# Optimization experiments

Hardware: AMD Instinct MI355X
Metric: run time of the kernel (lower is better)

The kernel has to match this reference:

```python
import math
import jax, jax.numpy as jnp
import numpy as np

B, L, D, H, DK = 2, 2048, 1024, 16, 64
LATTICE = (4, 4)


def _build_neighbours(n_heads, shape):
    positions = [divmod(i, shape[1]) for i in range(n_heads)]
    idx = np.full((n_heads, 8), -1, dtype=np.int32)
    w = np.zeros((n_heads, 8), dtype=np.float32)
    for i, (r1, c1) in enumerate(positions):
        k = 0
        for dr in (-1, 0, 1):
            for dc in (-1, 0, 1):
                if dr == 0 and dc == 0:
                    continue
                if k >= 8:
                    break
                tgt = (r1 + dr, c1 + dc)
                for j, p in enumerate(positions):
                    if p == tgt:
                        idx[i, k] = j
                        w[i, k] = math.exp(-math.hypot(dr, dc))
                        k += 1
                        break
    return idx, w


def setup_inputs() -> dict:
    key = jax.random.key(0)
    ks = jax.random.split(key, 8)
    s = 1.0 / math.sqrt(D)  # typical linear init scale
    nb_idx, nb_w = _build_neighbours(H, LATTICE)
    return {
        "query": jax.random.normal(ks[0], (B, L, D), jnp.float32),
        "key": jax.random.normal(ks[1], (B, L, D), jnp.float32),
        "value": jax.random.normal(ks[2], (B, L, D), jnp.float32),
        "Wq": jax.random.normal(ks[3], (H, DK, D), jnp.float32) * s,
        "Wk": jax.random.normal(ks[4], (H, DK, D), jnp.float32) * s,
        "Wv": jax.random.normal(ks[5], (H, DK, D), jnp.float32) * s,
        "coupling_strength": jnp.full((H,), 0.1, jnp.float32),
        "out_w": jax.random.normal(ks[6], (D, D), jnp.float32) * s,
        "out_b": jnp.zeros((D,), jnp.float32),
        "neighbour_w": jnp.asarray(nb_w),
        "mask": jax.random.randint(ks[7], (B, L), 0, 2, jnp.int32),
        "neighbour_idx": jnp.asarray(nb_idx),
    }


def _phases(coupling_strength, neighbour_idx, neighbour_w):
    # Sequential Kuramoto update over heads (order matters: earlier heads'
    # updated phases are visible to later heads, as in the torch loop).
    freq = 1.0 + 0.1 * jnp.arange(H, dtype=jnp.float32)
    ph = jnp.zeros((H,), jnp.float32)
    two_pi = 2.0 * math.pi
    for i in range(H):  # H=16, structurally distinct sequential states
        nb = jnp.clip(neighbour_idx[i], 0, H - 1)  # invalid slots have w==0
        coupling = jnp.sum(neighbour_w[i] * jnp.sin(ph[nb] - ph[i]))
        new = jnp.mod(ph[i] + 0.01 * (freq[i] + coupling_strength[i] * coupling), two_pi)
        ph = ph.at[i].set(new)
    return ph


def reference(query, key, value, Wq, Wk, Wv, coupling_strength, out_w, out_b,
              neighbour_w, mask, neighbour_idx):
    ph = _phases(coupling_strength, neighbour_idx, neighbour_w)
    bias = 0.1 * jnp.cos(ph)  # [H] per-head scalar bias

    # Batched per-head projections: [B,L,D] x [H,DK,D] -> [B,H,L,DK]
    Q = jnp.einsum('bld,hkd->bhlk', query, Wq)
    K = jnp.einsum('bld,hkd->bhlk', key, Wk)
    V = jnp.einsum('bld,hkd->bhlk', value, Wv)

    scale = math.sqrt(float(DK))
    scores = jnp.einsum('bhqd,bhkd->bhqk', Q, K) / scale  # [B,H,L,L]
    scores = scores + bias[None, :, None, None]
    m = mask[:, None, None, :]  # [B,1,1,L], matches mask.unsqueeze(1).unsqueeze(1)
    scores = jnp.where(m == 0, jnp.float32(-10000.0), scores)
    attn = jax.nn.softmax(scores, axis=-1)
    out = jnp.einsum('bhqk,bhkd->bhqd', attn, V)  # [B,H,L,DK]
    out = out.transpose(0, 2, 1, 3).reshape(B, L, H * DK)  # concat heads
    return out @ out_w.T + out_b
```

## Files before the change

### kernel.cpp

```cpp
#include <hip/hip_runtime.h>
#include <hip/hip_fp16.h>


#define B_ 2
#define L_ 2048
#define D_ 1024
#define H_ 16
#define DK_ 64

#define QSCALE 0.1803368801111244f
#define MASKOFF -14427.0f

typedef _Float16 f16;
typedef _Float16 f16x2 __attribute__((ext_vector_type(2)));
typedef _Float16 f16x4 __attribute__((ext_vector_type(4)));
typedef _Float16 f16x8 __attribute__((ext_vector_type(8)));
typedef __fp16 hf16x2 __attribute__((ext_vector_type(2)));
typedef float f32x4 __attribute__((ext_vector_type(4)));

static __device__ __forceinline__ float fast_exp2(float x) {
    float r;
    asm("v_exp_f32 %0, %1" : "=v"(r) : "v"(x));
    return r;
}

__global__ __launch_bounds__(256) void qkv_proj_kernel(
    const float* __restrict__ query, const float* __restrict__ keyx,
    const float* __restrict__ value,
    const float* __restrict__ Wq, const float* __restrict__ Wk,
    const float* __restrict__ Wv,
    f16* __restrict__ Qh, f16* __restrict__ Kh, f16* __restrict__ VhT)
{
    const int z = blockIdx.z;
    const float* X = (z == 0) ? query : (z == 1) ? keyx : value;
    const float* W = (z == 0) ? Wq : (z == 1) ? Wk : Wv;
    f16* out = (z == 0) ? Qh : (z == 1) ? Kh : VhT;
    const float qs = (z == 0) ? QSCALE : 1.0f;

    const int m0 = blockIdx.x * 128;
    const int n0 = blockIdx.y * 128;
    const int tid = threadIdx.x;
    const int lane = tid & 63;
    const int w = tid >> 6;
    const int wr = (w >> 1) * 64, wc = (w & 1) * 64;

    __shared__ f16 As[128 * 40];
    __shared__ f16 Ws[128 * 40];

    f32x4 acc[4][4] = {};

    const int r = tid >> 3, c = (tid & 7) * 4;
    float4 ra[4], rb[4];

    auto issueK = [&](int kk) {
        #pragma unroll
        for (int p = 0; p < 4; ++p) {
            ra[p] = *(const float4*)&X[(size_t)(m0 + p * 32 + r) * D_ + kk + c];
            rb[p] = *(const float4*)&W[(size_t)(n0 + p * 32 + r) * D_ + kk + c];
        }
    };
    auto storeK = [&]() {
        #pragma unroll
        for (int p = 0; p < 4; ++p) {
            int row = p * 32 + r;
            f16x4 ha = { (f16)(ra[p].x * qs), (f16)(ra[p].y * qs),
                         (f16)(ra[p].z * qs), (f16)(ra[p].w * qs) };
            *(f16x4*)&As[row * 40 + c] = ha;
            f16x4 hb = { (f16)rb[p].x, (f16)rb[p].y, (f16)rb[p].z, (f16)rb[p].w };
            *(f16x4*)&Ws[row * 40 + c] = hb;
        }
    };

    issueK(0);
    for (int kk = 0; kk < D_; kk += 32) {
        __syncthreads();
        storeK();
        if (kk + 32 < D_) issueK(kk + 32);
        __syncthreads();

        f16x8 af[4], bf[4];
        const int lg = (lane >> 4) * 8;
        #pragma unroll
        for (int i = 0; i < 4; ++i) {
            af[i] = *(const f16x8*)&As[(wr + i * 16 + (lane & 15)) * 40 + lg];
            bf[i] = *(const f16x8*)&Ws[(wc + i * 16 + (lane & 15)) * 40 + lg];
        }
        #pragma unroll
        for (int i = 0; i < 4; ++i)
            #pragma unroll
            for (int j = 0; j < 4; ++j)
                acc[i][j] = __builtin_amdgcn_mfma_f32_16x16x32_f16(af[i], bf[j], acc[i][j], 0, 0, 0);
    }

    if (z == 2) {
        #pragma unroll
        for (int i = 0; i < 4; ++i) {
            int grow = m0 + wr + i * 16 + (lane >> 4) * 4;
            int b = grow >> 11, l = grow & (L_ - 1);
            #pragma unroll
            for (int j = 0; j < 4; ++j) {
                int gcol = n0 + wc + j * 16 + (lane & 15);
                int hh = gcol >> 6, k = gcol & 63;
                f16x4 o = { (f16)acc[i][j][0], (f16)acc[i][j][1],
                            (f16)acc[i][j][2], (f16)acc[i][j][3] };
                *(f16x4*)&out[((size_t)((b * H_ + hh) * DK_ + k)) * L_ + l] = o;
            }
        }
    } else {
        #pragma unroll
        for (int i = 0; i < 4; ++i) {
            int grow = m0 + wr + i * 16 + (lane >> 4) * 4;
            #pragma unroll
            for (int j = 0; j < 4; ++j) {
                int gcol = n0 + wc + j * 16 + (lane & 15);
                int hh = gcol >> 6, k = gcol & 63;
                #pragma unroll
                for (int rr = 0; rr < 4; ++rr) {
                    int row = grow + rr;
                    int b = row >> 11, l = row & (L_ - 1);
                    out[(((size_t)(b * H_ + hh)) * L_ + l) * DK_ + k] = (f16)acc[i][j][rr];
                }
            }
        }
    }
}

__global__ __launch_bounds__(256) void attn_kernel(
    const f16* __restrict__ Qh, const f16* __restrict__ Kh,
    const f16* __restrict__ VhT, const int* __restrict__ mask,
    f16* __restrict__ Oh)
{
    const int n = blockIdx.x;
    const int bh = ((n >> 7) << 3) + (n & 7);
    const int qb = (n >> 3) & 15;
    const int b = bh >> 4, h = bh & 15;
    const int q0 = qb * 128;
    const int tid = threadIdx.x;
    const int lane = tid & 63;
    const int w = tid >> 6;
    const int lq = lane & 15, g = lane >> 4;

    __shared__ f16 Ks[2][64 * 72];
    __shared__ f16 Vt[2][64 * 72];
    __shared__ f16 Plds[4][32 * 72];
    __shared__ float mofft[2][64];

    const size_t base = (size_t)bh * L_ * DK_;
    const int* maskp = mask + b * L_;

    f16x8 qf0[2], qf1[2];
    {
        const f16* qptr = Qh + base + (size_t)(q0 + w * 32 + lq) * DK_ + g * 8;
        qf0[0] = *(const f16x8*)(qptr);
        qf0[1] = *(const f16x8*)(qptr + 32);
        qptr += 16 * DK_;
        qf1[0] = *(const f16x8*)(qptr);
        qf1[1] = *(const f16x8*)(qptr + 32);
    }

    const int srow = tid >> 2, scol = (tid & 3) * 16;

    f32x4 acc0[4] = {}, acc1[4] = {};
    float mrun0 = -1e30f, lrun0 = 0.f;
    float mrun1 = -1e30f, lrun1 = 0.f;

    f16x8 kr0, kr1, vr0, vr1;

    auto issue = [&](int k0) {
        const f16* kp = Kh + base + (size_t)(k0 + srow) * DK_ + scol;
        kr0 = *(const f16x8*)kp;
        kr1 = *(const f16x8*)(kp + 8);
        const f16* vp = VhT + (size_t)(bh * DK_ + srow) * L_ + k0 + scol;
        vr0 = *(const f16x8*)vp;
        vr1 = *(const f16x8*)(vp + 8);
    };

    auto store_tile = [&](int buf, int k0) {
        *(f16x8*)&Ks[buf][srow * 72 + scol] = kr0;
        *(f16x8*)&Ks[buf][srow * 72 + scol + 8] = kr1;
        *(f16x8*)&Vt[buf][srow * 72 + scol] = vr0;
        *(f16x8*)&Vt[buf][srow * 72 + scol + 8] = vr1;
        if (tid < 16) {
            int4 mv = *(const int4*)&maskp[k0 + tid * 4];
            float4 f = { mv.x ? 0.f : MASKOFF, mv.y ? 0.f : MASKOFF,
                         mv.z ? 0.f : MASKOFF, mv.w ? 0.f : MASKOFF };
            *(float4*)&mofft[buf][tid * 4] = f;
        }
    };

    auto softmax_store = [&](float* sv, float& mrun, float& lrun,
                             f32x4* acc, int rowoff) {
        float a0 = fmaxf(sv[0], sv[1]),  a1 = fmaxf(sv[2], sv[3]);
        float a2 = fmaxf(sv[4], sv[5]),  a3 = fmaxf(sv[6], sv[7]);
        float a4 = fmaxf(sv[8], sv[9]),  a5 = fmaxf(sv[10], sv[11]);
        float a6 = fmaxf(sv[12], sv[13]), a7 = fmaxf(sv[14], sv[15]);
        float m = fmaxf(fmaxf(fmaxf(a0, a1), fmaxf(a2, a3)),
                        fmaxf(fmaxf(a4, a5), fmaxf(a6, a7)));
        m = fmaxf(m, __shfl_xor(m, 16, 64));
        m = fmaxf(m, __shfl_xor(m, 32, 64));
        if (__any(m > mrun)) {
            float mn = fmaxf(mrun, m);
            float scl = fast_exp2(mrun - mn);
            mrun = mn;
            lrun *= scl;
            #pragma unroll
            for (int f = 0; f < 4; ++f) acc[f] *= scl;
        }
        f16* pl = (f16*)Plds[w];
        float ls0 = 0.f, ls1 = 0.f;
        #pragma unroll
        for (int kt = 0; kt < 4; ++kt) {
            float p0 = fast_exp2(sv[kt * 4 + 0] - mrun);
            float p1 = fast_exp2(sv[kt * 4 + 1] - mrun);
            float p2 = fast_exp2(sv[kt * 4 + 2] - mrun);
            float p3 = fast_exp2(sv[kt * 4 + 3] - mrun);
            ls0 += p0 + p1;
            ls1 += p2 + p3;
            hf16x2 lo = __builtin_amdgcn_cvt_pkrtz(p0, p1);
            hf16x2 hi = __builtin_amdgcn_cvt_pkrtz(p2, p3);
            f16x2 lo2 = __builtin_bit_cast(f16x2, lo);
            f16x2 hi2 = __builtin_bit_cast(f16x2, hi);
            f16x4 pk; pk[0] = lo2[0]; pk[1] = lo2[1]; pk[2] = hi2[0]; pk[3] = hi2[1];
            *(f16x4*)&pl[(rowoff + lq) * 72 + kt * 16 + g * 4] = pk;
        }
        lrun += ls0 + ls1;
    };

    auto compute = [&](int buf) {
        float sv0[16], sv1[16];
        __builtin_amdgcn_s_setprio(1);
        #pragma unroll
        for (int kt = 0; kt < 4; ++kt) {
            f32x4 cin = *(const f32x4*)&mofft[buf][kt * 16 + g * 4];
            const f16* ka = &Ks[buf][(kt * 16 + lq) * 72 + g * 8];
            f16x8 a0 = *(const f16x8*)ka;
            f16x8 a1 = *(const f16x8*)(ka + 32);
            f32x4 s0 = __builtin_amdgcn_mfma_f32_16x16x32_f16(a0, qf0[0], cin, 0, 0, 0);
            s0 = __builtin_amdgcn_mfma_f32_16x16x32_f16(a1, qf0[1], s0, 0, 0, 0);
            f32x4 s1 = __builtin_amdgcn_mfma_f32_16x16x32_f16(a0, qf1[0], cin, 0, 0, 0);
            s1 = __builtin_amdgcn_mfma_f32_16x16x32_f16(a1, qf1[1], s1, 0, 0, 0);
            *(f32x4*)&sv0[kt * 4] = s0;
            *(f32x4*)&sv1[kt * 4] = s1;
        }
        __builtin_amdgcn_s_setprio(0);

        softmax_store(sv0, mrun0, lrun0, acc0, 0);
        softmax_store(sv1, mrun1, lrun1, acc1, 16);
        asm volatile("s_waitcnt lgkmcnt(0)" ::: "memory");
        __builtin_amdgcn_sched_barrier(0);

        f16* pl = (f16*)Plds[w];
        __builtin_amdgcn_s_setprio(1);
        #pragma unroll
        for (int kc = 0; kc < 2; ++kc) {
            f16x8 pb0 = *(const f16x8*)&pl[lq * 72 + kc * 32 + g * 8];
            f16x8 pb1 = *(const f16x8*)&pl[(16 + lq) * 72 + kc * 32 + g * 8];
            #pragma unroll
            for (int f = 0; f < 4; ++f) {
                f16x8 va = *(const f16x8*)&Vt[buf][(f * 16 + lq) * 72 + kc * 32 + g * 8];
                acc0[f] = __builtin_amdgcn_mfma_f32_16x16x32_f16(va, pb0, acc0[f], 0, 0, 0);
                acc1[f] = __builtin_amdgcn_mfma_f32_16x16x32_f16(va, pb1, acc1[f], 0, 0, 0);
            }
        }
        __builtin_amdgcn_s_setprio(0);
    };

    issue(0);
    store_tile(0, 0);
    issue(64);
    __syncthreads();

    #pragma unroll 2
    for (int t = 0; t < 32; ++t) {
        int buf = t & 1;
        if (t + 1 < 32) store_tile(buf ^ 1, (t + 1) * 64);
        if (t + 2 < 32) issue((t + 2) * 64);
        compute(buf);
        __syncthreads();
    }

    lrun0 += __shfl_xor(lrun0, 16, 64);
    lrun0 += __shfl_xor(lrun0, 32, 64);
    lrun1 += __shfl_xor(lrun1, 16, 64);
    lrun1 += __shfl_xor(lrun1, 32, 64);
    {
        float inv = 1.f / lrun0;
        int q = q0 + w * 32 + lq;
        #pragma unroll
        for (int f = 0; f < 4; ++f) {
            f16x4 o = { (f16)(acc0[f][0] * inv), (f16)(acc0[f][1] * inv),
                        (f16)(acc0[f][2] * inv), (f16)(acc0[f][3] * inv) };
            *(f16x4*)&Oh[((size_t)(b * L_ + q)) * D_ + h * 64 + f * 16 + g * 4] = o;
        }
    }
    {
        float inv = 1.f / lrun1;
        int q = q0 + w * 32 + 16 + lq;
        #pragma unroll
        for (int f = 0; f < 4; ++f) {
            f16x4 o = { (f16)(acc1[f][0] * inv), (f16)(acc1[f][1] * inv),
                        (f16)(acc1[f][2] * inv), (f16)(acc1[f][3] * inv) };
            *(f16x4*)&Oh[((size_t)(b * L_ + q)) * D_ + h * 64 + f * 16 + g * 4] = o;
        }
    }
}

__global__ __launch_bounds__(256) void out_proj_kernel(
    const f16* __restrict__ Oh, const float* __restrict__ outw,
    const float* __restrict__ outb, float* __restrict__ Y)
{
    const int m0 = blockIdx.x * 128;
    const int n0 = blockIdx.y * 128;
    const int tid = threadIdx.x;
    const int lane = tid & 63;
    const int w = tid >> 6;
    const int wr = (w >> 1) * 64, wc = (w & 1) * 64;

    __shared__ f16 As[128 * 40];
    __shared__ f16 Ws[128 * 40];

    f32x4 acc[4][4] = {};

    const int r = tid >> 3, c = (tid & 7) * 4;
    f16x4 ra[4];
    float4 rb[4];

    auto issueK = [&](int kk) {
        #pragma unroll
        for (int p = 0; p < 4; ++p) {
            ra[p] = *(const f16x4*)&Oh[(size_t)(m0 + p * 32 + r) * D_ + kk + c];
            rb[p] = *(const float4*)&outw[(size_t)(n0 + p * 32 + r) * D_ + kk + c];
        }
    };
    auto storeK = [&]() {
        #pragma unroll
        for (int p = 0; p < 4; ++p) {
            int row = p * 32 + r;
            *(f16x4*)&As[row * 40 + c] = ra[p];
            f16x4 hb = { (f16)rb[p].x, (f16)rb[p].y, (f16)rb[p].z, (f16)rb[p].w };
            *(f16x4*)&Ws[row * 40 + c] = hb;
        }
    };

    issueK(0);
    for (int kk = 0; kk < D_; kk += 32) {
        __syncthreads();
        storeK();
        if (kk + 32 < D_) issueK(kk + 32);
        __syncthreads();

        f16x8 af[4], bf[4];
        const int lg = (lane >> 4) * 8;
        #pragma unroll
        for (int i = 0; i < 4; ++i) {
            af[i] = *(const f16x8*)&As[(wr + i * 16 + (lane & 15)) * 40 + lg];
            bf[i] = *(const f16x8*)&Ws[(wc + i * 16 + (lane & 15)) * 40 + lg];
        }
        #pragma unroll
        for (int i = 0; i < 4; ++i)
            #pragma unroll
            for (int j = 0; j < 4; ++j)
                acc[i][j] = __builtin_amdgcn_mfma_f32_16x16x32_f16(af[i], bf[j], acc[i][j], 0, 0, 0);
    }

    #pragma unroll
    for (int i = 0; i < 4; ++i) {
        int grow = m0 + wr + i * 16 + (lane >> 4) * 4;
        #pragma unroll
        for (int j = 0; j < 4; ++j) {
            int gcol = n0 + wc + j * 16 + (lane & 15);
            float bias = outb[gcol];
            #pragma unroll
            for (int rr = 0; rr < 4; ++rr)
                Y[(size_t)(grow + rr) * D_ + gcol] = acc[i][j][rr] + bias;
        }
    }
}

extern "C" void kernel_launch(void* const* d_in, const int* in_sizes, int n_in,
                              void* d_out, int out_size, void* d_ws, size_t ws_size,
                              hipStream_t stream) {
    const float* query = (const float*)d_in[0];
    const float* key   = (const float*)d_in[1];
    const float* value = (const float*)d_in[2];
    const float* Wq    = (const float*)d_in[3];
    const float* Wk    = (const float*)d_in[4];
    const float* Wv    = (const float*)d_in[5];
    const float* outw  = (const float*)d_in[7];
    const float* outb  = (const float*)d_in[8];
    const int*   mask  = (const int*)d_in[10];
    float* Y = (float*)d_out;

    char* ws = (char*)d_ws;
    f16* Qh  = (f16*)(ws);
    f16* Kh  = (f16*)(ws + 8388608);
    f16* VhT = (f16*)(ws + 16777216);
    f16* Oh  = (f16*)(ws + 25165824);

    qkv_proj_kernel<<<dim3(32, 8, 3), 256, 0, stream>>>(query, key, value,
                                                        Wq, Wk, Wv, Qh, Kh, VhT);
    attn_kernel<<<dim3(512), 256, 0, stream>>>(Qh, Kh, VhT, mask, Oh);
    out_proj_kernel<<<dim3(32, 8), 256, 0, stream>>>(Oh, outw, outb, Y);
}
```

Baseline: 149.9 us.

## Double-buffer LDS in projection GEMMs and swap MFMA operands for vector stores

The QKV projection and output projection GEMMs now use two LDS buffers, so each k-step needs one barrier instead of two and the next tile's store overlaps the current compute. The MFMA operands are swapped for row-major outputs, which transposes the accumulator layout so each lane holds four consecutive columns. The epilogue can then write f16x4 or float4 vectors instead of scalar stores. The cost is twice the LDS per block, which may lower occupancy.

After: 154.8 us. 1.03x slower.

```diff
diff --git a/kernel.cpp b/kernel.cpp
--- a/kernel.cpp
+++ b/kernel.cpp
@@ -44,8 +44,8 @@
     const int w = tid >> 6;
     const int wr = (w >> 1) * 64, wc = (w & 1) * 64;
 
-    __shared__ f16 As[128 * 40];
-    __shared__ f16 Ws[128 * 40];
+    __shared__ f16 As[2][128 * 40];
+    __shared__ f16 Ws[2][128 * 40];
 
     f32x4 acc[4][4] = {};
 
@@ -59,37 +59,52 @@
             rb[p] = *(const float4*)&W[(size_t)(n0 + p * 32 + r) * D_ + kk + c];
         }
     };
-    auto storeK = [&]() {
+    auto storeK = [&](int buf) {
         #pragma unroll
         for (int p = 0; p < 4; ++p) {
             int row = p * 32 + r;
             f16x4 ha = { (f16)(ra[p].x * qs), (f16)(ra[p].y * qs),
                          (f16)(ra[p].z * qs), (f16)(ra[p].w * qs) };
-            *(f16x4*)&As[row * 40 + c] = ha;
+            *(f16x4*)&As[buf][row * 40 + c] = ha;
             f16x4 hb = { (f16)rb[p].x, (f16)rb[p].y, (f16)rb[p].z, (f16)rb[p].w };
-            *(f16x4*)&Ws[row * 40 + c] = hb;
-        }
-    };
-
-    issueK(0);
-    for (int kk = 0; kk < D_; kk += 32) {
-        __syncthreads();
-        storeK();
-        if (kk + 32 < D_) issueK(kk + 32);
-        __syncthreads();
-
+            *(f16x4*)&Ws[buf][row * 40 + c] = hb;
+        }
+    };
+
+    auto computeK = [&](int buf) {
         f16x8 af[4], bf[4];
         const int lg = (lane >> 4) * 8;
         #pragma unroll
         for (int i = 0; i < 4; ++i) {
-            af[i] = *(const f16x8*)&As[(wr + i * 16 + (lane & 15)) * 40 + lg];
-            bf[i] = *(const f16x8*)&Ws[(wc + i * 16 + (lane & 15)) * 40 + lg];
-        }
-        #pragma unroll
-        for (int i = 0; i < 4; ++i)
-            #pragma unroll
-            for (int j = 0; j < 4; ++j)
-                acc[i][j] = __builtin_amdgcn_mfma_f32_16x16x32_f16(af[i], bf[j], acc[i][j], 0, 0, 0);
+            af[i] = *(const f16x8*)&As[buf][(wr + i * 16 + (lane & 15)) * 40 + lg];
+            bf[i] = *(const f16x8*)&Ws[buf][(wc + i * 16 + (lane & 15)) * 40 + lg];
+        }
+        if (z == 2) {
+            #pragma unroll
+            for (int i = 0; i < 4; ++i)
+                #pragma unroll
+                for (int j = 0; j < 4; ++j)
+                    acc[i][j] = __builtin_amdgcn_mfma_f32_16x16x32_f16(af[i], bf[j], acc[i][j], 0, 0, 0);
+        } else {
+            #pragma unroll
+            for (int i = 0; i < 4; ++i)
+                #pragma unroll
+                for (int j = 0; j < 4; ++j)
+                    acc[i][j] = __builtin_amdgcn_mfma_f32_16x16x32_f16(bf[j], af[i], acc[i][j], 0, 0, 0);
+        }
+    };
+
+    issueK(0);
+    storeK(0);
+    issueK(32);
+    __syncthreads();
+
+    for (int t = 0; t < 32; ++t) {
+        int buf = t & 1;
+        if (t + 1 < 32) storeK(buf ^ 1);
+        if (t + 2 < 32) issueK((t + 2) * 32);
+        computeK(buf);
+        __syncthreads();
     }
 
     if (z == 2) {
@@ -109,17 +124,15 @@
     } else {
         #pragma unroll
         for (int i = 0; i < 4; ++i) {
-            int grow = m0 + wr + i * 16 + (lane >> 4) * 4;
+            int m = m0 + wr + i * 16 + (lane & 15);
+            int b = m >> 11, l = m & (L_ - 1);
             #pragma unroll
             for (int j = 0; j < 4; ++j) {
-                int gcol = n0 + wc + j * 16 + (lane & 15);
-                int hh = gcol >> 6, k = gcol & 63;
-                #pragma unroll
-                for (int rr = 0; rr < 4; ++rr) {
-                    int row = grow + rr;
-                    int b = row >> 11, l = row & (L_ - 1);
-                    out[(((size_t)(b * H_ + hh)) * L_ + l) * DK_ + k] = (f16)acc[i][j][rr];
-                }
+                int nn = n0 + wc + j * 16 + (lane >> 4) * 4;
+                int hh = nn >> 6, k = nn & 63;
+                f16x4 o = { (f16)acc[i][j][0], (f16)acc[i][j][1],
+                            (f16)acc[i][j][2], (f16)acc[i][j][3] };
+                *(f16x4*)&out[(((size_t)(b * H_ + hh)) * L_ + l) * DK_ + k] = o;
             }
         }
     }
@@ -316,8 +329,8 @@
     const int w = tid >> 6;
     const int wr = (w >> 1) * 64, wc = (w & 1) * 64;
 
-    __shared__ f16 As[128 * 40];
-    __shared__ f16 Ws[128 * 40];
+    __shared__ f16 As[2][128 * 40];
+    __shared__ f16 Ws[2][128 * 40];
 
     f32x4 acc[4][4] = {};
 
@@ -332,47 +345,54 @@
             rb[p] = *(const float4*)&outw[(size_t)(n0 + p * 32 + r) * D_ + kk + c];
         }
     };
-    auto storeK = [&]() {
+    auto storeK = [&](int buf) {
         #pragma unroll
         for (int p = 0; p < 4; ++p) {
             int row = p * 32 + r;
-            *(f16x4*)&As[row * 40 + c] = ra[p];
+            *(f16x4*)&As[buf][row * 40 + c] = ra[p];
             f16x4 hb = { (f16)rb[p].x, (f16)rb[p].y, (f16)rb[p].z, (f16)rb[p].w };
-            *(f16x4*)&Ws[row * 40 + c] = hb;
-        }
-    };
-
-    issueK(0);
-    for (int kk = 0; kk < D_; kk += 32) {
-        __syncthreads();
-        storeK();
-        if (kk + 32 < D_) issueK(kk + 32);
-        __syncthreads();
-
+            *(f16x4*)&Ws[buf][row * 40 + c] = hb;
+        }
+    };
+
+    auto computeK = [&](int buf) {
         f16x8 af[4], bf[4];
         const int lg = (lane >> 4) * 8;
         #pragma unroll
         for (int i = 0; i < 4; ++i) {
-            af[i] = *(const f16x8*)&As[(wr + i * 16 + (lane & 15)) * 40 + lg];
-            bf[i] = *(const f16x8*)&Ws[(wc + i * 16 + (lane & 15)) * 40 + lg];
+            af[i] = *(const f16x8*)&As[buf][(wr + i * 16 + (lane & 15)) * 40 + lg];
+            bf[i] = *(const f16x8*)&Ws[buf][(wc + i * 16 + (lane & 15)) * 40 + lg];
         }
         #pragma unroll
         for (int i = 0; i < 4; ++i)
             #pragma unroll
             for (int j = 0; j < 4; ++j)
-                acc[i][j] = __builtin_amdgcn_mfma_f32_16x16x32_f16(af[i], bf[j], acc[i][j], 0, 0, 0);
+                acc[i][j] = __builtin_amdgcn_mfma_f32_16x16x32_f16(bf[j], af[i], acc[i][j], 0, 0, 0);
+    };
+
+    issueK(0);
+    storeK(0);
+    issueK(32);
+    __syncthreads();
+
+    for (int t = 0; t < 32; ++t) {
+        int buf = t & 1;
+        if (t + 1 < 32) storeK(buf ^ 1);
+        if (t + 2 < 32) issueK((t + 2) * 32);
+        computeK(buf);
+        __syncthreads();
     }
 
     #pragma unroll
     for (int i = 0; i < 4; ++i) {
-        int grow = m0 + wr + i * 16 + (lane >> 4) * 4;
+        int m = m0 + wr + i * 16 + (lane & 15);
         #pragma unroll
         for (int j = 0; j < 4; ++j) {
-            int gcol = n0 + wc + j * 16 + (lane & 15);
-            float bias = outb[gcol];
-            #pragma unroll
-            for (int rr = 0; rr < 4; ++rr)
-                Y[(size_t)(grow + rr) * D_ + gcol] = acc[i][j][rr] + bias;
+            int nn = n0 + wc + j * 16 + (lane >> 4) * 4;
+            float4 bias = *(const float4*)&outb[nn];
+            float4 o = { acc[i][j][0] + bias.x, acc[i][j][1] + bias.y,
+                         acc[i][j][2] + bias.z, acc[i][j][3] + bias.w };
+            *(float4*)&Y[(size_t)m * D_ + nn] = o;
         }
     }
 }
```

## Pre-convert inputs and weights to fp16 and use direct-to-LDS GEMM loads

Applied to the files above, without the earlier changes.

Adds separate kernels that convert the fp32 query/key/value activations and all projection weights to fp16 in workspace, applying the Q scale during conversion. New QKV and output projection GEMMs then stream fp16 tiles straight into swizzled, double-buffered LDS via global_load_lds, without register staging and in-loop conversion. The aim is to cut GEMM load and conversion overhead, at the cost of an extra full read and write pass over the activations. The path runs only when the workspace is at least 64 MiB; otherwise the old fp32-input kernels are used.

New measurement: 166.2 us. 1.11x slower.

```diff
diff --git a/kernel.cpp b/kernel.cpp
--- a/kernel.cpp
+++ b/kernel.cpp
@@ -24,7 +24,225 @@
     return r;
 }
 
-__global__ __launch_bounds__(256) void qkv_proj_kernel(
+static __device__ __forceinline__ void gload_lds16(const f16* g, f16* l) {
+    __builtin_amdgcn_global_load_lds(
+        (const __attribute__((address_space(1))) void*)g,
+        (__attribute__((address_space(3))) void*)l, 16, 0, 0);
+}
+
+static __device__ __forceinline__ f16x4 pack4(float a, float b, float c, float d) {
+    hf16x2 lo = __builtin_amdgcn_cvt_pkrtz(a, b);
+    hf16x2 hi = __builtin_amdgcn_cvt_pkrtz(c, d);
+    f16x2 l2 = __builtin_bit_cast(f16x2, lo);
+    f16x2 h2 = __builtin_bit_cast(f16x2, hi);
+    f16x4 o; o[0] = l2[0]; o[1] = l2[1]; o[2] = h2[0]; o[3] = h2[1];
+    return o;
+}
+
+__global__ __launch_bounds__(256) void conv_x_kernel(
+    const float* __restrict__ query, const float* __restrict__ keyx,
+    const float* __restrict__ value, f16* __restrict__ Xf)
+{
+    const int z = blockIdx.y;
+    const float* src = (z == 0) ? query : (z == 1) ? keyx : value;
+    const float s = (z == 0) ? QSCALE : 1.0f;
+    size_t i = ((size_t)blockIdx.x * 256 + threadIdx.x) * 8;
+    float4 a = *(const float4*)&src[i];
+    float4 b = *(const float4*)&src[i + 4];
+    f16x4 lo = pack4(a.x * s, a.y * s, a.z * s, a.w * s);
+    f16x4 hi = pack4(b.x * s, b.y * s, b.z * s, b.w * s);
+    f16x8 o; o[0]=lo[0]; o[1]=lo[1]; o[2]=lo[2]; o[3]=lo[3];
+    o[4]=hi[0]; o[5]=hi[1]; o[6]=hi[2]; o[7]=hi[3];
+    *(f16x8*)&Xf[(size_t)z * 4194304 + i] = o;
+}
+
+__global__ __launch_bounds__(256) void conv_w_kernel(
+    const float* __restrict__ Wq, const float* __restrict__ Wk,
+    const float* __restrict__ Wv, const float* __restrict__ outw,
+    f16* __restrict__ Wf)
+{
+    const int z = blockIdx.y;
+    const float* src = (z == 0) ? Wq : (z == 1) ? Wk : (z == 2) ? Wv : outw;
+    size_t i = ((size_t)blockIdx.x * 256 + threadIdx.x) * 8;
+    float4 a = *(const float4*)&src[i];
+    float4 b = *(const float4*)&src[i + 4];
+    f16x4 lo = pack4(a.x, a.y, a.z, a.w);
+    f16x4 hi = pack4(b.x, b.y, b.z, b.w);
+    f16x8 o; o[0]=lo[0]; o[1]=lo[1]; o[2]=lo[2]; o[3]=lo[3];
+    o[4]=hi[0]; o[5]=hi[1]; o[6]=hi[2]; o[7]=hi[3];
+    *(f16x8*)&Wf[(size_t)z * 1048576 + i] = o;
+}
+
+
+__global__ __launch_bounds__(256) void qkv_proj_f16_kernel(
+    const f16* __restrict__ Xf, const f16* __restrict__ Wf,
+    f16* __restrict__ Qh, f16* __restrict__ Kh, f16* __restrict__ VhT)
+{
+    const int z = blockIdx.z;
+    const f16* A = Xf + (size_t)z * 4194304;
+    const f16* Bm = Wf + (size_t)z * 1048576;
+    f16* out = (z == 0) ? Qh : (z == 1) ? Kh : VhT;
+
+    const int m0 = blockIdx.x * 128;
+    const int n0 = blockIdx.y * 128;
+    const int tid = threadIdx.x;
+    const int lane = tid & 63;
+    const int w = tid >> 6;
+    const int wr = (w >> 1) * 64, wc = (w & 1) * 64;
+    const int lq = lane & 15, g = lane >> 4;
+
+    __shared__ f16 As[2][4096];
+    __shared__ f16 Ws[2][4096];
+
+    f32x4 acc[4][4] = {};
+
+    const int srow = (lane >> 2);
+    const int slin = lane & 3;
+
+    auto stage = [&](int buf, int kk) {
+        #pragma unroll
+        for (int cc = 0; cc < 2; ++cc) {
+            int ch = w * 2 + cc;
+            int row = ch * 16 + srow;
+            int c8 = slin ^ ((row >> 1) & 3);
+            gload_lds16(&A[(size_t)(m0 + row) * 1024 + kk + c8 * 8], &As[buf][ch * 512]);
+            gload_lds16(&Bm[(size_t)(n0 + row) * 1024 + kk + c8 * 8], &Ws[buf][ch * 512]);
+        }
+    };
+
+    auto compute = [&](int buf) {
+        f16x8 af[4], bf[4];
+        #pragma unroll
+        for (int i = 0; i < 4; ++i) {
+            int R = wr + i * 16 + lq;
+            af[i] = *(const f16x8*)&As[buf][R * 32 + (g ^ ((R >> 1) & 3)) * 8];
+            int Rb = wc + i * 16 + lq;
+            bf[i] = *(const f16x8*)&Ws[buf][Rb * 32 + (g ^ ((Rb >> 1) & 3)) * 8];
+        }
+        if (z == 2) {
+            #pragma unroll
+            for (int i = 0; i < 4; ++i)
+                #pragma unroll
+                for (int j = 0; j < 4; ++j)
+                    acc[i][j] = __builtin_amdgcn_mfma_f32_16x16x32_f16(af[i], bf[j], acc[i][j], 0, 0, 0);
+        } else {
+            #pragma unroll
+            for (int i = 0; i < 4; ++i)
+                #pragma unroll
+                for (int j = 0; j < 4; ++j)
+                    acc[i][j] = __builtin_amdgcn_mfma_f32_16x16x32_f16(bf[j], af[i], acc[i][j], 0, 0, 0);
+        }
+    };
+
+    stage(0, 0);
+    for (int t = 0; t < 32; ++t) {
+        int buf = t & 1;
+        __syncthreads();
+        if (t + 1 < 32) stage(buf ^ 1, (t + 1) * 32);
+        compute(buf);
+    }
+
+    if (z == 2) {
+        #pragma unroll
+        for (int i = 0; i < 4; ++i) {
+            int grow = m0 + wr + i * 16 + (lane >> 4) * 4;
+            int b = grow >> 11, l = grow & (L_ - 1);
+            #pragma unroll
+            for (int j = 0; j < 4; ++j) {
+                int gcol = n0 + wc + j * 16 + (lane & 15);
+                int hh = gcol >> 6, k = gcol & 63;
+                f16x4 o = { (f16)acc[i][j][0], (f16)acc[i][j][1],
+                            (f16)acc[i][j][2], (f16)acc[i][j][3] };
+                *(f16x4*)&out[((size_t)((b * H_ + hh) * DK_ + k)) * L_ + l] = o;
+            }
+        }
+    } else {
+        #pragma unroll
+        for (int i = 0; i < 4; ++i) {
+            int m = m0 + wr + i * 16 + (lane & 15);
+            int b = m >> 11, l = m & (L_ - 1);
+            #pragma unroll
+            for (int j = 0; j < 4; ++j) {
+                int nn = n0 + wc + j * 16 + (lane >> 4) * 4;
+                int hh = nn >> 6, k = nn & 63;
+                f16x4 o = { (f16)acc[i][j][0], (f16)acc[i][j][1],
+                            (f16)acc[i][j][2], (f16)acc[i][j][3] };
+                *(f16x4*)&out[(((size_t)(b * H_ + hh)) * L_ + l) * DK_ + k] = o;
+            }
+        }
+    }
+}
+
+__global__ __launch_bounds__(256) void out_proj_f16_kernel(
+    const f16* __restrict__ Oh, const f16* __restrict__ Wof,
+    const float* __restrict__ outb, float* __restrict__ Y)
+{
+    const int m0 = blockIdx.x * 128;
+    const int n0 = blockIdx.y * 128;
+    const int tid = threadIdx.x;
+    const int lane = tid & 63;
+    const int w = tid >> 6;
+    const int wr = (w >> 1) * 64, wc = (w & 1) * 64;
+    const int lq = lane & 15, g = lane >> 4;
+
+    __shared__ f16 As[2][4096];
+    __shared__ f16 Ws[2][4096];
+
+    f32x4 acc[4][4] = {};
+
+    const int srow = (lane >> 2);
+    const int slin = lane & 3;
+
+    auto stage = [&](int buf, int kk) {
+        #pragma unroll
+        for (int cc = 0; cc < 2; ++cc) {
+            int ch = w * 2 + cc;
+            int row = ch * 16 + srow;
+            int c8 = slin ^ ((row >> 1) & 3);
+            gload_lds16(&Oh[(size_t)(m0 + row) * 1024 + kk + c8 * 8], &As[buf][ch * 512]);
+            gload_lds16(&Wof[(size_t)(n0 + row) * 1024 + kk + c8 * 8], &Ws[buf][ch * 512]);
+        }
+    };
+
+    auto compute = [&](int buf) {
+        f16x8 af[4], bf[4];
+        #pragma unroll
+        for (int i = 0; i < 4; ++i) {
+            int R = wr + i * 16 + lq;
+            af[i] = *(const f16x8*)&As[buf][R * 32 + (g ^ ((R >> 1) & 3)) * 8];
+            int Rb = wc + i * 16 + lq;
+            bf[i] = *(const f16x8*)&Ws[buf][Rb * 32 + (g ^ ((Rb >> 1) & 3)) * 8];
+        }
+        #pragma unroll
+        for (int i = 0; i < 4; ++i)
+            #pragma unroll
+            for (int j = 0; j < 4; ++j)
+                acc[i][j] = __builtin_amdgcn_mfma_f32_16x16x32_f16(bf[j], af[i], acc[i][j], 0, 0, 0);
+    };
+
+    stage(0, 0);
+    for (int t = 0; t < 32; ++t) {
+        int buf = t & 1;
+        __syncthreads();
+        if (t + 1 < 32) stage(buf ^ 1, (t + 1) * 32);
+        compute(buf);
+    }
+
+    #pragma unroll
+    for (int i = 0; i < 4; ++i) {
+        int m = m0 + wr + i * 16 + (lane & 15);
+        #pragma unroll
+        for (int j = 0; j < 4; ++j) {
+            int nn = n0 + wc + j * 16 + (lane >> 4) * 4;
+            float4 bias = *(const float4*)&outb[nn];
+            float4 o = { acc[i][j][0] + bias.x, acc[i][j][1] + bias.y,
+                         acc[i][j][2] + bias.z, acc[i][j][3] + bias.w };
+            *(float4*)&Y[(size_t)m * D_ + nn] = o;
+        }
+    }
+}
+
+__global__ __launch_bounds__(256) void qkv_proj_f32_kernel(
     const float* __restrict__ query, const float* __restrict__ keyx,
     const float* __restrict__ value,
     const float* __restrict__ Wq, const float* __restrict__ Wk,
@@ -121,6 +339,78 @@
                     out[(((size_t)(b * H_ + hh)) * L_ + l) * DK_ + k] = (f16)acc[i][j][rr];
                 }
             }
+        }
+    }
+}
+
+__global__ __launch_bounds__(256) void out_proj_f32_kernel(
+    const f16* __restrict__ Oh, const float* __restrict__ outw,
+    const float* __restrict__ outb, float* __restrict__ Y)
+{
+    const int m0 = blockIdx.x * 128;
+    const int n0 = blockIdx.y * 128;
+    const int tid = threadIdx.x;
+    const int lane = tid & 63;
+    const int w = tid >> 6;
+    const int wr = (w >> 1) * 64, wc = (w & 1) * 64;
+
+    __shared__ f16 As[128 * 40];
+    __shared__ f16 Ws[128 * 40];
+
+    f32x4 acc[4][4] = {};
+
+    const int r = tid >> 3, c = (tid & 7) * 4;
+    f16x4 ra[4];
+    float4 rb[4];
+
+    auto issueK = [&](int kk) {
+        #pragma unroll
+        for (int p = 0; p < 4; ++p) {
+            ra[p] = *(const f16x4*)&Oh[(size_t)(m0 + p * 32 + r) * D_ + kk + c];
+            rb[p] = *(const float4*)&outw[(size_t)(n0 + p * 32 + r) * D_ + kk + c];
+        }
+    };
+    auto storeK = [&]() {
+        #pragma unroll
+        for (int p = 0; p < 4; ++p) {
+            int row = p * 32 + r;
+            *(f16x4*)&As[row * 40 + c] = ra[p];
+            f16x4 hb = { (f16)rb[p].x, (f16)rb[p].y, (f16)rb[p].z, (f16)rb[p].w };
+            *(f16x4*)&Ws[row * 40 + c] = hb;
+        }
+    };
+
+    issueK(0);
+    for (int kk = 0; kk < D_; kk += 32) {
+        __syncthreads();
+        storeK();
+        if (kk + 32 < D_) issueK(kk + 32);
+        __syncthreads();
+
+        f16x8 af[4], bf[4];
+        const int lg = (lane >> 4) * 8;
+        #pragma unroll
+        for (int i = 0; i < 4; ++i) {
+            af[i] = *(const f16x8*)&As[(wr + i * 16 + (lane & 15)) * 40 + lg];
+            bf[i] = *(const f16x8*)&Ws[(wc + i * 16 + (lane & 15)) * 40 + lg];
+        }
+        #pragma unroll
+        for (int i = 0; i < 4; ++i)
+            #pragma unroll
+            for (int j = 0; j < 4; ++j)
+                acc[i][j] = __builtin_amdgcn_mfma_f32_16x16x32_f16(af[i], bf[j], acc[i][j], 0, 0, 0);
+    }
+
+    #pragma unroll
+    for (int i = 0; i < 4; ++i) {
+        int grow = m0 + wr + i * 16 + (lane >> 4) * 4;
+        #pragma unroll
+        for (int j = 0; j < 4; ++j) {
+            int gcol = n0 + wc + j * 16 + (lane & 15);
+            float bias = outb[gcol];
+            #pragma unroll
+            for (int rr = 0; rr < 4; ++rr)
+                Y[(size_t)(grow + rr) * D_ + gcol] = acc[i][j][rr] + bias;
         }
     }
 }
@@ -216,11 +506,7 @@
             float p3 = fast_exp2(sv[kt * 4 + 3] - mrun);
             ls0 += p0 + p1;
             ls1 += p2 + p3;
-            hf16x2 lo = __builtin_amdgcn_cvt_pkrtz(p0, p1);
-            hf16x2 hi = __builtin_amdgcn_cvt_pkrtz(p2, p3);
-            f16x2 lo2 = __builtin_bit_cast(f16x2, lo);
-            f16x2 hi2 = __builtin_bit_cast(f16x2, hi);
-            f16x4 pk; pk[0] = lo2[0]; pk[1] = lo2[1]; pk[2] = hi2[0]; pk[3] = hi2[1];
+            f16x4 pk = pack4(p0, p1, p2, p3);
             *(f16x4*)&pl[(rowoff + lq) * 72 + kt * 16 + g * 4] = pk;
         }
         lrun += ls0 + ls1;
@@ -301,78 +587,6 @@
             f16x4 o = { (f16)(acc1[f][0] * inv), (f16)(acc1[f][1] * inv),
                         (f16)(acc1[f][2] * inv), (f16)(acc1[f][3] * inv) };
             *(f16x4*)&Oh[((size_t)(b * L_ + q)) * D_ + h * 64 + f * 16 + g * 4] = o;
-        }
-    }
-}
-
-__global__ __launch_bounds__(256) void out_proj_kernel(
-    const f16* __restrict__ Oh, const float* __restrict__ outw,
-    const float* __restrict__ outb, float* __restrict__ Y)
-{
-    const int m0 = blockIdx.x * 128;
-    const int n0 = blockIdx.y * 128;
-    const int tid = threadIdx.x;
-    const int lane = tid & 63;
-    const int w = tid >> 6;
-    const int wr = (w >> 1) * 64, wc = (w & 1) * 64;
-
-    __shared__ f16 As[128 * 40];
-    __shared__ f16 Ws[128 * 40];
-
-    f32x4 acc[4][4] = {};
-
-    const int r = tid >> 3, c = (tid & 7) * 4;
-    f16x4 ra[4];
-    float4 rb[4];
-
-    auto issueK = [&](int kk) {
-        #pragma unroll
-        for (int p = 0; p < 4; ++p) {
-            ra[p] = *(const f16x4*)&Oh[(size_t)(m0 + p * 32 + r) * D_ + kk + c];
-            rb[p] = *(const float4*)&outw[(size_t)(n0 + p * 32 + r) * D_ + kk + c];
-        }
-    };
-    auto storeK = [&]() {
-        #pragma unroll
-        for (int p = 0; p < 4; ++p) {
-            int row = p * 32 + r;
-            *(f16x4*)&As[row * 40 + c] = ra[p];
-            f16x4 hb = { (f16)rb[p].x, (f16)rb[p].y, (f16)rb[p].z, (f16)rb[p].w };
-            *(f16x4*)&Ws[row * 40 + c] = hb;
-        }
-    };
-
-    issueK(0);
-    for (int kk = 0; kk < D_; kk += 32) {
-        __syncthreads();
-        storeK();
-        if (kk + 32 < D_) issueK(kk + 32);
-        __syncthreads();
-
-        f16x8 af[4], bf[4];
-        const int lg = (lane >> 4) * 8;
-        #pragma unroll
-        for (int i = 0; i < 4; ++i) {
-            af[i] = *(const f16x8*)&As[(wr + i * 16 + (lane & 15)) * 40 + lg];
-            bf[i] = *(const f16x8*)&Ws[(wc + i * 16 + (lane & 15)) * 40 + lg];
-        }
-        #pragma unroll
-        for (int i = 0; i < 4; ++i)
-            #pragma unroll
-            for (int j = 0; j < 4; ++j)
-                acc[i][j] = __builtin_amdgcn_mfma_f32_16x16x32_f16(af[i], bf[j], acc[i][j], 0, 0, 0);
-    }
-
-    #pragma unroll
-    for (int i = 0; i < 4; ++i) {
-        int grow = m0 + wr + i * 16 + (lane >> 4) * 4;
-        #pragma unroll
-        for (int j = 0; j < 4; ++j) {
-            int gcol = n0 + wc + j * 16 + (lane & 15);
-            float bias = outb[gcol];
-            #pragma unroll
-            for (int rr = 0; rr < 4; ++rr)
-                Y[(size_t)(grow + rr) * D_ + gcol] = acc[i][j][rr] + bias;
         }
     }
 }
@@ -397,8 +611,22 @@
     f16* VhT = (f16*)(ws + 16777216);
     f16* Oh  = (f16*)(ws + 25165824);
 
-    qkv_proj_kernel<<<dim3(32, 8, 3), 256, 0, stream>>>(query, key, value,
-                                                        Wq, Wk, Wv, Qh, Kh, VhT);
-    attn_kernel<<<dim3(512), 256, 0, stream>>>(Qh, Kh, VhT, mask, Oh);
-    out_proj_kernel<<<dim3(32, 8), 256, 0, stream>>>(Oh, outw, outb, Y);
-}
+    const bool fat = ws_size >= 67108864ull;
+
+    if (fat) {
+        f16* Xf = (f16*)(ws + 33554432);
+        f16* Wf = (f16*)(ws + 58720256);
+
+        conv_x_kernel<<<dim3(2048, 3), 256, 0, stream>>>(query, key, value, Xf);
+        conv_w_kernel<<<dim3(512, 4), 256, 0, stream>>>(Wq, Wk, Wv, outw, Wf);
+        qkv_proj_f16_kernel<<<dim3(32, 8, 3), 256, 0, stream>>>(Xf, Wf, Qh, Kh, VhT);
+        attn_kernel<<<dim3(512), 256, 0, stream>>>(Qh, Kh, VhT, mask, Oh);
+        out_proj_f16_kernel<<<dim3(32, 8), 256, 0, stream>>>(
+            Oh, Wf + (size_t)3 * 1048576, outb, Y);
+    } else {
+        qkv_proj_f32_kernel<<<dim3(32, 8, 3), 256, 0, stream>>>(query, key, value,
+                                                                Wq, Wk, Wv, Qh, Kh, VhT);
+        attn_kernel<<<dim3(512), 256, 0, stream>>>(Qh, Kh, VhT, mask, Oh);
+        out_proj_f32_kernel<<<dim3(32, 8), 256, 0, stream>>>(Oh, outw, outb, Y);
+    }
+}
```
